# Kernel optimization log

Measured on AMD Instinct MI355X. Metric: run time of the kernel, lower is better.

The kernel has to match this reference:

```python
import jax, jax.numpy as jnp
import numpy as np

B, C, N, H = 4, 512, 2048, 8
D = C // H  # per-head depth = 64
EPS = 1e-5


def conv1x1(x, W, b):
    # x: [B, Cin, N], W: [Cout, Cin], b: [Cout]
    return jnp.einsum('oc,bcn->bon', W, x) + b[None, :, None]


def instance_norm(x):
    # normalize over length dim per (batch, channel), no affine
    mu = jnp.mean(x, axis=-1, keepdims=True)
    var = jnp.var(x, axis=-1, keepdims=True)
    return (x - mu) * jax.lax.rsqrt(var + EPS)


def _pipeline(src, tgt, Wq, bq, Wk, bk, Wv, bv, Wm, bm):
    # query from src, key/value from tgt; reshape C -> (D outer, H inner)
    q = conv1x1(src, Wq, bq).reshape(B, D, H, N)
    k = conv1x1(tgt, Wk, bk).reshape(B, D, H, N)
    v = conv1x1(tgt, Wv, bv).reshape(B, D, H, N)
    scores = jnp.einsum('bdhn,bdhm->bhnm', q, k) / jnp.sqrt(jnp.float32(D))
    probs = jax.nn.softmax(scores, axis=-1)
    out = jnp.einsum('bhnm,bdhm->bdhn', probs, v).reshape(B, C, N)
    return conv1x1(out, Wm, bm)


def _mlp(x, W1, b1, W2, b2):
    h = conv1x1(x, W1, b1)
    h = jax.nn.relu(instance_norm(h))
    return conv1x1(h, W2, b2)


def setup_inputs() -> dict:
    key = jax.random.key(0)
    ks = jax.random.split(key, 8)
    s = 0.02
    return {
        'source_features': jax.random.normal(ks[0], (B, C, N), jnp.float32),
        'target_features': jax.random.normal(ks[1], (B, C, N), jnp.float32),
        'Wq': jax.random.normal(ks[2], (C, C), jnp.float32) * s,
        'bq': jnp.zeros((C,), jnp.float32),
        'Wk': jax.random.normal(ks[3], (C, C), jnp.float32) * s,
        'bk': jnp.zeros((C,), jnp.float32),
        'Wv': jax.random.normal(ks[4], (C, C), jnp.float32) * s,
        'bv': jnp.zeros((C,), jnp.float32),
        'Wm': jax.random.normal(ks[5], (C, C), jnp.float32) * s,
        'bm': jnp.zeros((C,), jnp.float32),
        'W1': jax.random.normal(ks[6], (2 * C, 2 * C), jnp.float32) * s,
        'b1': jnp.zeros((2 * C,), jnp.float32),
        'W2': jax.random.normal(ks[7], (C, 2 * C), jnp.float32) * s,
        'b2': jnp.zeros((C,), jnp.float32),
    }


def reference(source_features, target_features, Wq, bq, Wk, bk, Wv, bv, Wm, bm, W1, b1, W2, b2):
    src, tgt = source_features, target_features
    # source update uses ORIGINAL target features
    src_att = _pipeline(src, tgt, Wq, bq, Wk, bk, Wv, bv, Wm, bm)
    src = src + _mlp(jnp.concatenate([src, src_att], axis=1), W1, b1, W2, b2)
    # target update uses the UPDATED source features (in-place semantics of original)
    tgt_att = _pipeline(tgt, src, Wq, bq, Wk, bk, Wv, bv, Wm, bm)
    tgt = tgt + _mlp(jnp.concatenate([tgt, tgt_att], axis=1), W1, b1, W2, b2)
    return src, tgt
```

## Files before the change

kernel.cpp:

```cpp
#include <hip/hip_runtime.h>

#define NN 2048
#define CC 512
#define BB 4
#define HH 8
#define DD 64
#define SCALE 0.18033688011112043f

typedef unsigned short u16;
typedef __attribute__((ext_vector_type(8))) short bf16x8;
typedef __attribute__((ext_vector_type(4))) float f32x4;

extern "C" __device__ float __ocml_exp2_f32(float);

__device__ inline u16 f2b(float x) {
    unsigned u = __builtin_bit_cast(unsigned, x);
    u += 0x7fffu + ((u >> 16) & 1u);
    return (u16)(u >> 16);
}
__device__ inline float b2f(u16 h) {
    unsigned u = ((unsigned)h) << 16;
    return __builtin_bit_cast(float, u);
}

#define GLD16(g, l) __builtin_amdgcn_global_load_lds( \
    (const __attribute__((address_space(1))) unsigned int*)(g), \
    (__attribute__((address_space(3))) unsigned int*)(l), 16, 0, 0)

template<int JT>
__device__ __forceinline__ void gemm_core_t(
    const u16* __restrict__ Xa, const u16* __restrict__ Xb, int Ca, int K,
    const u16* __restrict__ Wt, size_t rowBase,
    u16* As, u16* Bs, f32x4 (&acc)[4][JT])
{
    constexpr int OT = JT * 32;
    const int tid = threadIdx.x;
    const int lane = tid & 63, w = tid >> 6;
    const int quad = lane >> 4, l16 = lane & 15;
    const int wrow = w & 1, wcol = w >> 1;
    const int arow = lane >> 2, aseg = lane & 3;

    for (int k0 = 0; k0 < K; k0 += 32) {
        const u16* Xs; int Crow, cc;
        if (k0 < Ca) { Xs = Xa; Crow = Ca; cc = k0; }
        else         { Xs = Xb; Crow = K - Ca; cc = k0 - Ca; }
#pragma unroll
        for (int i = 0; i < 2; ++i) {
            int rl = w * 32 + i * 16 + arow;
            int la = __builtin_amdgcn_readfirstlane((w * 32 + i * 16) * 32);
            GLD16(Xs + (rowBase + rl) * (size_t)Crow + cc + aseg * 8, (char*)As + (size_t)la * 2);
        }
#pragma unroll
        for (int i = 0; i < OT / 64; ++i) {
            int rl = w * (OT / 4) + i * 16 + arow;
            int la = __builtin_amdgcn_readfirstlane((w * (OT / 4) + i * 16) * 32);
            GLD16(Wt + (size_t)rl * K + k0 + aseg * 8, (char*)Bs + (size_t)la * 2);
        }
        __syncthreads();
        bf16x8 av[4], bv[JT];
#pragma unroll
        for (int i = 0; i < 4; ++i)
            av[i] = *(const bf16x8*)&As[(wrow * 64 + i * 16 + l16) * 32 + quad * 8];
#pragma unroll
        for (int jj = 0; jj < JT; ++jj)
            bv[jj] = *(const bf16x8*)&Bs[(wcol * JT * 16 + jj * 16 + l16) * 32 + quad * 8];
#pragma unroll
        for (int i = 0; i < 4; ++i)
#pragma unroll
            for (int jj = 0; jj < JT; ++jj)
                acc[i][jj] = __builtin_amdgcn_mfma_f32_16x16x32_bf16(av[i], bv[jj], acc[i][jj], 0, 0, 0);
        __syncthreads();
    }
}

template<int JT>
__device__ __forceinline__ void gemm_epilogue_t(
    f32x4 (&acc)[4][JT], const float* __restrict__ bias, int mode,
    int b, int n0, int o0, int Cout,
    const float* __restrict__ res, float* __restrict__ outF, u16* __restrict__ outB)
{
    const int tid = threadIdx.x;
    const int lane = tid & 63, w = tid >> 6;
    const int quad = lane >> 4, l16 = lane & 15;
    const int wrow = w & 1, wcol = w >> 1;
    const size_t bN = (size_t)b * NN;
    const int nb0 = n0 + wrow * 64, ob0 = o0 + wcol * JT * 16;

    if (mode == 0) {
#pragma unroll
        for (int j = 0; j < JT; ++j) {
            int o = ob0 + j * 16 + l16;
            float bs = bias[o];
#pragma unroll
            for (int i = 0; i < 4; ++i)
#pragma unroll
                for (int r = 0; r < 4; ++r) {
                    int n = nb0 + i * 16 + quad * 4 + r;
                    outB[(bN + n) * Cout + o] = f2b(acc[i][j][r] + bs);
                }
        }
    } else if (mode == 1) {
#pragma unroll
        for (int j = 0; j < JT; ++j) {
            int o = ob0 + j * 16 + l16;
            float bs = bias[o];
            int h = o >> 6, d = o & 63;
#pragma unroll
            for (int i = 0; i < 4; ++i) {
                int n = nb0 + i * 16 + quad * 4;
                ushort4 pk;
                pk.x = f2b(acc[i][j][0] + bs); pk.y = f2b(acc[i][j][1] + bs);
                pk.z = f2b(acc[i][j][2] + bs); pk.w = f2b(acc[i][j][3] + bs);
                *(ushort4*)&outB[(((size_t)b * HH + h) * DD + d) * NN + n] = pk;
            }
        }
    } else {
#pragma unroll
        for (int j = 0; j < JT; ++j) {
            int o = ob0 + j * 16 + l16;
            float bs = bias[o];
#pragma unroll
            for (int i = 0; i < 4; ++i) {
                int n = nb0 + i * 16 + quad * 4;
                size_t ad = ((size_t)b * Cout + o) * NN + n;
                float4 rv = *(const float4*)&res[ad];
                float4 yv;
                yv.x = acc[i][j][0] + bs + rv.x;
                yv.y = acc[i][j][1] + bs + rv.y;
                yv.z = acc[i][j][2] + bs + rv.z;
                yv.w = acc[i][j][3] + bs + rv.w;
                *(float4*)&outF[ad] = yv;
                if (mode == 2) {
                    outB[(bN + n + 0) * Cout + o] = f2b(yv.x);
                    outB[(bN + n + 1) * Cout + o] = f2b(yv.y);
                    outB[(bN + n + 2) * Cout + o] = f2b(yv.z);
                    outB[(bN + n + 3) * Cout + o] = f2b(yv.w);
                }
            }
        }
    }
}

template<int JT>
__global__ __launch_bounds__(256, (JT == 2 ? 4 : 3)) void gemm_bf16_t(
    const u16* __restrict__ Wb, const float* __restrict__ bias,
    const u16* __restrict__ Xa, const u16* __restrict__ Xb,
    int Ca, int K, int Cout,
    const float* __restrict__ res, float* __restrict__ outF,
    u16* __restrict__ outB, int mode)
{
    __shared__ u16 As[128 * 32];
    __shared__ u16 Bs[JT * 32 * 32];
    const int b = blockIdx.z, n0 = blockIdx.x * 128, o0 = blockIdx.y * (JT * 32);
    f32x4 acc[4][JT] = {};
    gemm_core_t<JT>(Xa, Xb, Ca, K, Wb + (size_t)o0 * K, (size_t)b * NN + n0, As, Bs, acc);
    gemm_epilogue_t<JT>(acc, bias, mode, b, n0, o0, Cout, res, outF, outB);
}

__global__ __launch_bounds__(256, 3) void gemm_qkv(
    const u16* __restrict__ WQ, const float* __restrict__ bQ,
    const u16* __restrict__ XQ, u16* __restrict__ outQ,
    const u16* __restrict__ WK, const float* __restrict__ bK, u16* __restrict__ outK,
    const u16* __restrict__ WV, const float* __restrict__ bV, u16* __restrict__ outV,
    const u16* __restrict__ XKV)
{
    __shared__ u16 As[128 * 32];
    __shared__ u16 Bs[128 * 32];
    const int yb = blockIdx.y;
    const u16* W; const float* bias; const u16* X; u16* outB; int mode, o0;
    if (yb < 4)      { o0 = yb * 128;       W = WQ; bias = bQ; X = XQ;  outB = outQ; mode = 0; }
    else if (yb < 8) { o0 = (yb - 4) * 128; W = WK; bias = bK; X = XKV; outB = outK; mode = 0; }
    else             { o0 = (yb - 8) * 128; W = WV; bias = bV; X = XKV; outB = outV; mode = 1; }
    const int b = blockIdx.z, n0 = blockIdx.x * 128;
    f32x4 acc[4][4] = {};
    gemm_core_t<4>(X, nullptr, 512, 512, W + (size_t)o0 * 512, (size_t)b * NN + n0, As, Bs, acc);
    gemm_epilogue_t<4>(acc, bias, mode, b, n0, o0, 512, nullptr, nullptr, outB);
}

__global__ __launch_bounds__(256, 4) void attn(
    const u16* __restrict__ Qg, const u16* __restrict__ Kg,
    const u16* __restrict__ Vg, u16* __restrict__ Og)
{
    __shared__ __align__(16) u16 Ks[64 * 64];
    __shared__ __align__(16) u16 Vt[64 * 64];
    __shared__ __align__(16) u16 Ps[64 * 64];
    const int tid = threadIdx.x;
    const int lane = tid & 63, w = tid >> 6;
    const int quad = lane >> 4, l16 = lane & 15;
    const int id = blockIdx.x;
    const int xcd = id & 7, jj = id >> 3;
    const int bh = xcd * 4 + (jj >> 5), nb = jj & 31;
    const int b = bh >> 3, h = bh & 7;
    const int n0 = nb * 64, wn0 = w * 16;
    const size_t qkBase = ((size_t)b * NN) * CC + h * DD;
    const size_t vBase  = (((size_t)b * HH + h) * DD) * NN;
    const int r8 = lane >> 3, seg = lane & 7;
    const int lk = l16 & 7;

    bf16x8 qf[2];
    {
        int n = n0 + wn0 + l16;
#pragma unroll
        for (int ks = 0; ks < 2; ++ks)
            qf[ks] = *(const bf16x8*)&Qg[qkBase + (size_t)n * CC + ks * 32 + quad * 8];
    }

    const short oneb = 0x3F80;
    const bf16x8 ones = {oneb, oneb, oneb, oneb, oneb, oneb, oneb, oneb};
    f32x4 oa[4] = {};
    f32x4 lacc = {};

    for (int m0 = 0; m0 < NN; m0 += 64) {
#pragma unroll
        for (int it = 0; it < 2; ++it) {
            int rowb = w * 16 + it * 8;
            int segp = seg ^ r8;
            GLD16(&Kg[qkBase + (size_t)(m0 + rowb + r8) * CC + segp * 8], &Ks[rowb * 64]);
            GLD16(&Vg[vBase + (size_t)(rowb + r8) * NN + m0 + segp * 8], &Vt[rowb * 64]);
        }
        __syncthreads();

        f32x4 st[4] = {};
#pragma unroll
        for (int ks = 0; ks < 2; ++ks) {
            bf16x8 ak[4];
#pragma unroll
            for (int rt = 0; rt < 4; ++rt)
                ak[rt] = *(const bf16x8*)&Ks[(rt * 16 + l16) * 64 + ((ks * 4 + quad) ^ lk) * 8];
#pragma unroll
            for (int rt = 0; rt < 4; ++rt)
                st[rt] = __builtin_amdgcn_mfma_f32_16x16x32_bf16(ak[rt], qf[ks], st[rt], 0, 0, 0);
        }

        {
            int nrow = wn0 + l16;
#pragma unroll
            for (int rt = 0; rt < 4; ++rt) {
                unsigned u0 = __builtin_bit_cast(unsigned, __ocml_exp2_f32(st[rt][0]));
                unsigned u1 = __builtin_bit_cast(unsigned, __ocml_exp2_f32(st[rt][1]));
                unsigned u2 = __builtin_bit_cast(unsigned, __ocml_exp2_f32(st[rt][2]));
                unsigned u3 = __builtin_bit_cast(unsigned, __ocml_exp2_f32(st[rt][3]));
                uint2 t;
                t.x = __builtin_amdgcn_perm(u1, u0, 0x07060302u);
                t.y = __builtin_amdgcn_perm(u3, u2, 0x07060302u);
                int g = (rt * 2 + (quad >> 1)) ^ lk;
                *(uint2*)&Ps[nrow * 64 + g * 8 + (quad & 1) * 4] = t;
            }
        }

#pragma unroll
        for (int ks = 0; ks < 2; ++ks) {
            bf16x8 pa = *(const bf16x8*)&Ps[(wn0 + l16) * 64 + ((ks * 4 + quad) ^ lk) * 8];
            bf16x8 vb[4];
#pragma unroll
            for (int ct = 0; ct < 4; ++ct)
                vb[ct] = *(const bf16x8*)&Vt[(ct * 16 + l16) * 64 + ((ks * 4 + quad) ^ lk) * 8];
#pragma unroll
            for (int ct = 0; ct < 4; ++ct)
                oa[ct] = __builtin_amdgcn_mfma_f32_16x16x32_bf16(pa, vb[ct], oa[ct], 0, 0, 0);
            lacc = __builtin_amdgcn_mfma_f32_16x16x32_bf16(pa, ones, lacc, 0, 0, 0);
        }
        __syncthreads();
    }

#pragma unroll
    for (int r = 0; r < 4; ++r) {
        float li = 1.f / lacc[r];
        int n = n0 + wn0 + quad * 4 + r;
#pragma unroll
        for (int ct = 0; ct < 4; ++ct)
            Og[qkBase + (size_t)n * CC + ct * 16 + l16] = f2b(oa[ct][r] * li);
    }
}

__global__ __launch_bounds__(256) void transpose_cvt(
    const float* __restrict__ X, u16* __restrict__ Y)
{
    __shared__ float T[64][65];
    const int tid = threadIdx.x;
    const int n0 = blockIdx.x * 64, c0 = blockIdx.y * 64, b = blockIdx.z;
    const int rr = tid >> 4, cc4 = tid & 15;
#pragma unroll
    for (int p = 0; p < 4; ++p) {
        int cl = p * 16 + rr;
        float4 v = *(const float4*)&X[((size_t)b * CC + c0 + cl) * NN + n0 + cc4 * 4];
        T[cl][cc4 * 4 + 0] = v.x; T[cl][cc4 * 4 + 1] = v.y;
        T[cl][cc4 * 4 + 2] = v.z; T[cl][cc4 * 4 + 3] = v.w;
    }
    __syncthreads();
#pragma unroll
    for (int p = 0; p < 4; ++p) {
        int nl = p * 16 + rr;
        ushort4 pk;
        pk.x = f2b(T[cc4 * 4 + 0][nl]);
        pk.y = f2b(T[cc4 * 4 + 1][nl]);
        pk.z = f2b(T[cc4 * 4 + 2][nl]);
        pk.w = f2b(T[cc4 * 4 + 3][nl]);
        *(ushort4*)&Y[((size_t)b * NN + n0 + nl) * CC + c0 + cc4 * 4] = pk;
    }
}

__global__ __launch_bounds__(256) void prep_weights(
    const float* __restrict__ Wq, const float* __restrict__ Wk,
    const float* __restrict__ Wv, const float* __restrict__ Wm,
    const float* __restrict__ W1, const float* __restrict__ W2,
    u16* oQ, u16* oK, u16* oV, u16* oM, u16* o1, u16* o2)
{
    const float* W; u16* o; int rows, cols, perm; float sc = 1.f;
    switch (blockIdx.z) {
        case 0: W = Wq; o = oQ; rows = 512;  cols = 512;  perm = 1; sc = SCALE; break;
        case 1: W = Wk; o = oK; rows = 512;  cols = 512;  perm = 1; break;
        case 2: W = Wv; o = oV; rows = 512;  cols = 512;  perm = 1; break;
        case 3: W = Wm; o = oM; rows = 512;  cols = 512;  perm = 2; break;
        case 4: W = W1; o = o1; rows = 1024; cols = 1024; perm = 0; break;
        default: W = W2; o = o2; rows = 512; cols = 1024; perm = 0; break;
    }
    int c = blockIdx.x * 256 + threadIdx.x;
    int r = blockIdx.y;
    if (r >= rows || c >= cols) return;
    int sr = r, scol = c;
    if (perm == 1) sr = (r & 63) * 8 + (r >> 6);
    else if (perm == 2) scol = (c & 63) * 8 + (c >> 6);
    o[(size_t)r * cols + c] = f2b(W[(size_t)sr * cols + scol] * sc);
}

__global__ void prep_bias(const float* __restrict__ bq, const float* __restrict__ bk,
                          const float* __restrict__ bv,
                          float* oq, float* ok, float* ov)
{
    int i = blockIdx.x * 256 + threadIdx.x;
    int y = blockIdx.y;
    const float* s = (y == 0) ? bq : (y == 1) ? bk : bv;
    float* o = (y == 0) ? oq : (y == 1) ? ok : ov;
    float v = s[(i & 63) * 8 + (i >> 6)];
    if (y == 0) v *= SCALE;
    o[i] = v;
}

__global__ __launch_bounds__(256) void inorm_p1(
    const u16* __restrict__ X, float* __restrict__ Ssum, float* __restrict__ Ssq)
{
    __shared__ float rs[4][64], rq[4][64];
    const int tid = threadIdx.x;
    const int cl = tid & 63, g = tid >> 6;
    const int c = blockIdx.x * 64 + cl;
    const int b = blockIdx.y, nz = blockIdx.z;
    float s = 0.f, q = 0.f;
    size_t base = ((size_t)b * NN + nz * 256 + g * 64) * 1024 + c;
#pragma unroll 4
    for (int i = 0; i < 64; ++i) {
        float x = b2f(X[base + (size_t)i * 1024]);
        s += x; q += x * x;
    }
    rs[g][cl] = s; rq[g][cl] = q;
    __syncthreads();
    if (g == 0) {
        s = rs[0][cl] + rs[1][cl] + rs[2][cl] + rs[3][cl];
        q = rq[0][cl] + rq[1][cl] + rq[2][cl] + rq[3][cl];
        atomicAdd(&Ssum[b * 1024 + c], s);
        atomicAdd(&Ssq[b * 1024 + c], q);
    }
}

__global__ __launch_bounds__(256) void inorm_p2(
    u16* __restrict__ X, const float* __restrict__ Ssum, const float* __restrict__ Ssq)
{
    const int tid = threadIdx.x;
    const int cl = tid & 63, g = tid >> 6;
    const int c = blockIdx.x * 64 + cl;
    const int b = blockIdx.y, nz = blockIdx.z;
    float mean = Ssum[b * 1024 + c] * (1.f / NN);
    float var  = Ssq[b * 1024 + c] * (1.f / NN) - mean * mean;
    float rstd = rsqrtf(fmaxf(var, 0.f) + 1e-5f);
    size_t base = ((size_t)b * NN + nz * 256 + g * 64) * 1024 + c;
#pragma unroll 4
    for (int i = 0; i < 64; ++i) {
        float x = b2f(X[base + (size_t)i * 1024]);
        x = (x - mean) * rstd;
        X[base + (size_t)i * 1024] = f2b(fmaxf(x, 0.f));
    }
}

extern "C" void kernel_launch(void* const* d_in, const int* in_sizes, int n_in,
                              void* d_out, int out_size, void* d_ws, size_t ws_size,
                              hipStream_t stream)
{
    (void)in_sizes; (void)n_in; (void)out_size; (void)ws_size;
    const float* src = (const float*)d_in[0];
    const float* tgt = (const float*)d_in[1];
    const float* Wq = (const float*)d_in[2];  const float* bq = (const float*)d_in[3];
    const float* Wk = (const float*)d_in[4];  const float* bk = (const float*)d_in[5];
    const float* Wv = (const float*)d_in[6];  const float* bv = (const float*)d_in[7];
    const float* Wm = (const float*)d_in[8];  const float* bm = (const float*)d_in[9];
    const float* W1 = (const float*)d_in[10]; const float* b1 = (const float*)d_in[11];
    const float* W2 = (const float*)d_in[12]; const float* b2 = (const float*)d_in[13];

    char* w = (char*)d_ws;
    u16* WQp = (u16*)(w);
    u16* WKp = (u16*)(w + (512u << 10));
    u16* WVp = (u16*)(w + (1u << 20));
    u16* WMp = (u16*)(w + (3u << 19));
    u16* W1b = (u16*)(w + (2u << 20));
    u16* W2b = (u16*)(w + (4u << 20));
    float* BQp = (float*)(w + (5u << 20));
    float* BKp = BQp + 512;
    float* BVp = BQp + 1024;
    float* STS = BQp + 1536;
    float* STQ = STS + 4096;
    u16* X0 = (u16*)(w + ( 6u << 20));
    u16* X1 = (u16*)(w + (14u << 20));
    u16* B0 = (u16*)(w + (22u << 20));
    u16* B1 = (u16*)(w + (30u << 20));
    u16* B2 = (u16*)(w + (38u << 20));
    u16* B3 = (u16*)(w + (46u << 20));

    float* out = (float*)d_out;
    const size_t R = (size_t)BB * CC * NN;
    dim3 blk(256);

    prep_weights<<<dim3(4, 1024, 6), blk, 0, stream>>>(Wq, Wk, Wv, Wm, W1, W2,
                                                       WQp, WKp, WVp, WMp, W1b, W2b);
    prep_bias<<<dim3(2, 3), blk, 0, stream>>>(bq, bk, bv, BQp, BKp, BVp);
    transpose_cvt<<<dim3(32, 8, 4), blk, 0, stream>>>(src, X0);
    transpose_cvt<<<dim3(32, 8, 4), blk, 0, stream>>>(tgt, X1);

    dim3 gQKV(16, 12, 4), gM(16, 8, 4), gW1(16, 8, 4), gW2(16, 8, 4);

    gemm_qkv<<<gQKV, blk, 0, stream>>>(WQp, BQp, X0, B0, WKp, BKp, B1, WVp, BVp, B2, X1);
    attn<<<dim3(1024), blk, 0, stream>>>(B0, B1, B2, B3);
    gemm_bf16_t<2><<<gM, blk, 0, stream>>>(WMp, bm, B3, nullptr, 512, 512, 512, nullptr, nullptr, B0, 0);
    gemm_bf16_t<4><<<gW1, blk, 0, stream>>>(W1b, b1, X0, B0, 512, 1024, 1024, nullptr, nullptr, B1, 0);
    hipMemsetAsync(STS, 0, 8192 * sizeof(float), stream);
    inorm_p1<<<dim3(16, 4, 8), blk, 0, stream>>>(B1, STS, STQ);
    inorm_p2<<<dim3(16, 4, 8), blk, 0, stream>>>(B1, STS, STQ);
    gemm_bf16_t<2><<<gW2, blk, 0, stream>>>(W2b, b2, B1, nullptr, 1024, 1024, 512, src, out, B3, 2);

    gemm_qkv<<<gQKV, blk, 0, stream>>>(WQp, BQp, X1, X0, WKp, BKp, B0, WVp, BVp, B1, B3);
    attn<<<dim3(1024), blk, 0, stream>>>(X0, B0, B1, B2);
    gemm_bf16_t<2><<<gM, blk, 0, stream>>>(WMp, bm, B2, nullptr, 512, 512, 512, nullptr, nullptr, X0, 0);
    gemm_bf16_t<4><<<gW1, blk, 0, stream>>>(W1b, b1, X1, X0, 512, 1024, 1024, nullptr, nullptr, B0, 0);
    hipMemsetAsync(STS, 0, 8192 * sizeof(float), stream);
    inorm_p1<<<dim3(16, 4, 8), blk, 0, stream>>>(B0, STS, STQ);
    inorm_p2<<<dim3(16, 4, 8), blk, 0, stream>>>(B0, STS, STQ);
    gemm_bf16_t<2><<<gW2, blk, 0, stream>>>(W2b, b2, B0, nullptr, 1024, 1024, 512, tgt, out + R, nullptr, 3);
}
```

Measured before the change: 447.6 us.

## Double-buffer K/V tiles in attention to overlap loads with MFMA

Splits the attention kernel's K and V shared-memory tiles into two buffers. The next tile is prefetched while the current one is being computed, and one of the two per-iteration barriers is removed. The aim is to hide global-to-LDS load latency behind the QK and PV matrix work. In exchange, shared-memory use per block grows to about 40KB, which may press on the four-blocks-per-CU occupancy target.

```diff
diff --git a/kernel.cpp b/kernel.cpp
--- a/kernel.cpp
+++ b/kernel.cpp
@@ -181,8 +181,8 @@
     const u16* __restrict__ Qg, const u16* __restrict__ Kg,
     const u16* __restrict__ Vg, u16* __restrict__ Og)
 {
-    __shared__ __align__(16) u16 Ks[64 * 64];
-    __shared__ __align__(16) u16 Vt[64 * 64];
+    __shared__ __align__(16) u16 Ks[2][64 * 64];
+    __shared__ __align__(16) u16 Vt[2][64 * 64];
     __shared__ __align__(16) u16 Ps[64 * 64];
     const int tid = threadIdx.x;
     const int lane = tid & 63, w = tid >> 6;
@@ -195,7 +195,13 @@
     const size_t qkBase = ((size_t)b * NN) * CC + h * DD;
     const size_t vBase  = (((size_t)b * HH + h) * DD) * NN;
     const int r8 = lane >> 3, seg = lane & 7;
+    const int segp = seg ^ r8;
     const int lk = l16 & 7;
+
+    const u16* kp0 = Kg + qkBase + (size_t)(wn0 + r8) * CC + segp * 8;
+    const u16* kp1 = kp0 + (size_t)8 * CC;
+    const u16* vp0 = Vg + vBase + (size_t)(wn0 + r8) * NN + segp * 8;
+    const u16* vp1 = vp0 + (size_t)8 * NN;
 
     bf16x8 qf[2];
     {
@@ -210,15 +216,28 @@
     f32x4 oa[4] = {};
     f32x4 lacc = {};
 
-    for (int m0 = 0; m0 < NN; m0 += 64) {
-#pragma unroll
-        for (int it = 0; it < 2; ++it) {
-            int rowb = w * 16 + it * 8;
-            int segp = seg ^ r8;
-            GLD16(&Kg[qkBase + (size_t)(m0 + rowb + r8) * CC + segp * 8], &Ks[rowb * 64]);
-            GLD16(&Vg[vBase + (size_t)(rowb + r8) * NN + m0 + segp * 8], &Vt[rowb * 64]);
-        }
+    GLD16(kp0, &Ks[0][wn0 * 64]);
+    GLD16(kp1, &Ks[0][(wn0 + 8) * 64]);
+    GLD16(vp0, &Vt[0][wn0 * 64]);
+    GLD16(vp1, &Vt[0][(wn0 + 8) * 64]);
+    kp0 += 64 * CC; kp1 += 64 * CC; vp0 += 64; vp1 += 64;
+
+    for (int it = 0; it < NN / 64; ++it) {
+        const int cur = it & 1;
         __syncthreads();
+
+        if (it < NN / 64 - 1) {
+            u16* kd = Ks[cur ^ 1];
+            u16* vd = Vt[cur ^ 1];
+            GLD16(kp0, kd + wn0 * 64);
+            GLD16(kp1, kd + (wn0 + 8) * 64);
+            GLD16(vp0, vd + wn0 * 64);
+            GLD16(vp1, vd + (wn0 + 8) * 64);
+            kp0 += 64 * CC; kp1 += 64 * CC; vp0 += 64; vp1 += 64;
+        }
+
+        const u16* ksb = Ks[cur];
+        const u16* vtb = Vt[cur];
 
         f32x4 st[4] = {};
 #pragma unroll
@@ -226,7 +245,7 @@
             bf16x8 ak[4];
 #pragma unroll
             for (int rt = 0; rt < 4; ++rt)
-                ak[rt] = *(const bf16x8*)&Ks[(rt * 16 + l16) * 64 + ((ks * 4 + quad) ^ lk) * 8];
+                ak[rt] = *(const bf16x8*)&ksb[(rt * 16 + l16) * 64 + ((ks * 4 + quad) ^ lk) * 8];
 #pragma unroll
             for (int rt = 0; rt < 4; ++rt)
                 st[rt] = __builtin_amdgcn_mfma_f32_16x16x32_bf16(ak[rt], qf[ks], st[rt], 0, 0, 0);
@@ -254,13 +273,12 @@
             bf16x8 vb[4];
 #pragma unroll
             for (int ct = 0; ct < 4; ++ct)
-                vb[ct] = *(const bf16x8*)&Vt[(ct * 16 + l16) * 64 + ((ks * 4 + quad) ^ lk) * 8];
+                vb[ct] = *(const bf16x8*)&vtb[(ct * 16 + l16) * 64 + ((ks * 4 + quad) ^ lk) * 8];
 #pragma unroll
             for (int ct = 0; ct < 4; ++ct)
                 oa[ct] = __builtin_amdgcn_mfma_f32_16x16x32_bf16(pa, vb[ct], oa[ct], 0, 0, 0);
             lacc = __builtin_amdgcn_mfma_f32_16x16x32_bf16(pa, ones, lacc, 0, 0, 0);
         }
-        __syncthreads();
     }
 
 #pragma unroll
```

New measurement: 445.2 us. About the same (-0.5%).
